# Performance work log

Hardware: AMD Instinct MI355X
Metric: run time of the kernel (lower is better)

The kernel has to match this reference:

```python
import jax, jax.numpy as jnp
import numpy as np

B, N, C, H, D = 1, 256, 128, 4, 32  # batch, n_res, rep2d channels, heads, head dim


def setup_inputs() -> dict:
    key = jax.random.key(0)
    ks = jax.random.split(key, 8)
    r = lambda k, sh: jax.random.normal(k, sh, jnp.float32) * 0.02
    return {
        "x2d": jax.random.normal(ks[0], (B, N, N, C), jnp.float32),
        "norm_w": jnp.ones((C,), jnp.float32),
        "norm_b": jnp.zeros((C,), jnp.float32),
        "wq": r(ks[1], (H * D, C)),
        "wk": r(ks[2], (H * D, C)),
        "wv": r(ks[3], (H * D, C)),
        "wb": r(ks[4], (H, C)),
        "wg": r(ks[5], (H * D, C)),
        "bg": jnp.zeros((H * D,), jnp.float32),
        "wo": r(ks[6], (C, H * D)),
        "bo": jnp.zeros((C,), jnp.float32),
    }


def reference(x2d, norm_w, norm_b, wq, wk, wv, wb, wg, bg, wo, bo):
    # ending_node=False -> no transpose
    mu = jnp.mean(x2d, axis=-1, keepdims=True)
    var = jnp.var(x2d, axis=-1, keepdims=True)
    x = (x2d - mu) * jax.lax.rsqrt(var + 1e-5) * norm_w + norm_b  # LayerNorm

    q = (x @ wq.T).reshape(B, N, N, H, D)
    k = (x @ wk.T).reshape(B, N, N, H, D)
    v = (x @ wv.T).reshape(B, N, N, H, D)

    factor = 1.0 / np.sqrt(D)
    aff = jnp.einsum('bmihd,bmjhd->bmhij', q * factor, k)  # [B,M,H,I,J]

    bias = (x @ wb.T).transpose(0, 3, 1, 2)  # [B,H,I,J]
    # torch `aff + bias` broadcasts bias over the row dim m (valid since B==1)
    weights = jax.nn.softmax(aff + bias[:, None], axis=-1)

    g = jax.nn.sigmoid(x @ wg.T + bg).reshape(B, N, N, H, D)
    out = jnp.einsum('bmhqk,bmkhd->bmqhd', weights, v) * g  # gated per-head output
    out = out.reshape(B, N, N, H * D) @ wo.T + bo
    return out
```

## Files before the change

kernel.cpp:

```cpp
#include <hip/hip_runtime.h>
#include <hip/hip_bf16.h>

#define NRES 256
#define CH   128
#define NH   4
#define HD   32
#define NPX  (NRES*NRES)
#define BPX  64
#define LOG2E 1.4426950408889634f

typedef __hip_bfloat16 bf16;
typedef __attribute__((ext_vector_type(8))) short bf16x8;
typedef __attribute__((ext_vector_type(4))) float f32x4;
typedef __attribute__((ext_vector_type(16))) float f32x16;
typedef __attribute__((ext_vector_type(2))) unsigned int uint2v;

__device__ __forceinline__ float lo_f(unsigned u) { return __uint_as_float(u << 16); }
__device__ __forceinline__ float hi_f(unsigned u) { return __uint_as_float(u & 0xffff0000u); }
__device__ __forceinline__ float fexp2(float x) { return __builtin_amdgcn_exp2f(x); }
__device__ __forceinline__ unsigned pk2(float a, float b) {
    unsigned short ua = __bfloat16_as_ushort(__float2bfloat16(a));
    unsigned short ub = __bfloat16_as_ushort(__float2bfloat16(b));
    return (unsigned)ua | ((unsigned)ub << 16);
}

__global__ __launch_bounds__(256) void prep_kernel(const float* __restrict__ wq,
                                                   const float* __restrict__ wk,
                                                   const float* __restrict__ wv,
                                                   const float* __restrict__ wg,
                                                   const float* __restrict__ wo,
                                                   bf16* __restrict__ dst) {
    int mat = blockIdx.x >> 4;
    int off = ((blockIdx.x & 15) * 256 + threadIdx.x) * 4;
    const float* srcs[5] = {wq, wk, wv, wg, wo};
    float4 v4 = *reinterpret_cast<const float4*>(srcs[mat] + off);
    uint2 o;
    o.x = pk2(v4.x, v4.y);
    o.y = pk2(v4.z, v4.w);
    *reinterpret_cast<uint2*>(dst + (size_t)mat * 16384 + off) = o;
}

__global__ __launch_bounds__(256) void proj_kernel(const float* __restrict__ x2d,
                                                   const float* __restrict__ nw,
                                                   const float* __restrict__ nb,
                                                   const bf16* __restrict__ wgt,
                                                   const float* __restrict__ bg,
                                                   const float* __restrict__ wb,
                                                   bf16* __restrict__ q,
                                                   bf16* __restrict__ k,
                                                   bf16* __restrict__ v,
                                                   bf16* __restrict__ g,
                                                   float* __restrict__ bias) {
    __shared__ short xsb[BPX][128];
    int t = threadIdx.x;
    size_t pbase = (size_t)blockIdx.x * BPX;
    int px = t >> 2, lo = t & 3;

    const float* xrow = x2d + (pbase + px) * CH;
    float4 v4[8];
    #pragma unroll
    for (int cc = 0; cc < 8; ++cc)
        v4[cc] = *reinterpret_cast<const float4*>(xrow + 16 * cc + 4 * lo);

    float s = 0.f, ss = 0.f;
    #pragma unroll
    for (int cc = 0; cc < 8; ++cc) {
        s  += v4[cc].x + v4[cc].y + v4[cc].z + v4[cc].w;
        ss += v4[cc].x * v4[cc].x + v4[cc].y * v4[cc].y
            + v4[cc].z * v4[cc].z + v4[cc].w * v4[cc].w;
    }
    s += __shfl_xor(s, 1); ss += __shfl_xor(ss, 1);
    s += __shfl_xor(s, 2); ss += __shfl_xor(ss, 2);
    float mu  = s * (1.0f / CH);
    float var = ss * (1.0f / CH) - mu * mu;
    float rs  = rsqrtf(var + 1e-5f);

    #pragma unroll
    for (int cc = 0; cc < 8; ++cc) {
        int c0 = 16 * cc + 4 * lo;
        float4 wv = *reinterpret_cast<const float4*>(nw + c0);
        float4 bv = *reinterpret_cast<const float4*>(nb + c0);
        v4[cc].x = (v4[cc].x - mu) * rs * wv.x + bv.x;
        v4[cc].y = (v4[cc].y - mu) * rs * wv.y + bv.y;
        v4[cc].z = (v4[cc].z - mu) * rs * wv.z + bv.z;
        v4[cc].w = (v4[cc].w - mu) * rs * wv.w + bv.w;
        int sc = ((((c0 >> 3) ^ px) & 7) << 3) | (c0 & 7) | (c0 & 64);
        uint2 pw;
        pw.x = pk2(v4[cc].x, v4[cc].y);
        pw.y = pk2(v4[cc].z, v4[cc].w);
        *reinterpret_cast<uint2*>(&xsb[px][sc]) = pw;
    }

    float bp0 = 0.f, bp1 = 0.f, bp2 = 0.f, bp3 = 0.f;
    #pragma unroll
    for (int cc = 0; cc < 8; ++cc) {
        int c0 = 16 * cc + 4 * lo;
        float4 w0 = *reinterpret_cast<const float4*>(wb + 0 * CH + c0);
        float4 w1 = *reinterpret_cast<const float4*>(wb + 1 * CH + c0);
        float4 w2 = *reinterpret_cast<const float4*>(wb + 2 * CH + c0);
        float4 w3 = *reinterpret_cast<const float4*>(wb + 3 * CH + c0);
        bp0 += v4[cc].x * w0.x + v4[cc].y * w0.y + v4[cc].z * w0.z + v4[cc].w * w0.w;
        bp1 += v4[cc].x * w1.x + v4[cc].y * w1.y + v4[cc].z * w1.z + v4[cc].w * w1.w;
        bp2 += v4[cc].x * w2.x + v4[cc].y * w2.y + v4[cc].z * w2.z + v4[cc].w * w2.w;
        bp3 += v4[cc].x * w3.x + v4[cc].y * w3.y + v4[cc].z * w3.z + v4[cc].w * w3.w;
    }
    bp0 += __shfl_xor(bp0, 1); bp0 += __shfl_xor(bp0, 2);
    bp1 += __shfl_xor(bp1, 1); bp1 += __shfl_xor(bp1, 2);
    bp2 += __shfl_xor(bp2, 1); bp2 += __shfl_xor(bp2, 2);
    bp3 += __shfl_xor(bp3, 1); bp3 += __shfl_xor(bp3, 2);
    {
        float bv = (lo == 0) ? bp0 : (lo == 1) ? bp1 : (lo == 2) ? bp2 : bp3;
        bias[(size_t)lo * NPX + pbase + px] = bv * LOG2E;
    }
    __syncthreads();

    int w  = t >> 6, l = t & 63;
    int ll = l & 15, lg = l >> 4;
    bf16* Os[4] = {q, k, v, g};
    const float qscale = 0.17677669529663689f * LOG2E;

    #pragma unroll
    for (int mat = 0; mat < 4; ++mat) {
        const bf16* W = wgt + (size_t)mat * 16384;
        bf16x8 bfr[2][4];
        #pragma unroll
        for (int p = 0; p < 2; ++p)
            #pragma unroll
            for (int kt = 0; kt < 4; ++kt)
                bfr[p][kt] = *reinterpret_cast<const bf16x8*>(
                    W + (size_t)((2 * w + p) * 16 + ll) * CH + kt * 32 + lg * 8);

        f32x4 acc[4][2];
        #pragma unroll
        for (int mt = 0; mt < 4; ++mt)
            #pragma unroll
            for (int p = 0; p < 2; ++p) acc[mt][p] = (f32x4){0.f, 0.f, 0.f, 0.f};

        #pragma unroll
        for (int kt = 0; kt < 4; ++kt) {
            bf16x8 a[4];
            #pragma unroll
            for (int mt = 0; mt < 4; ++mt) {
                int row = 16 * mt + ll;
                int gr  = (kt * 4 + lg) ^ (row & 7);
                a[mt] = *reinterpret_cast<const bf16x8*>(&xsb[row][gr * 8]);
            }
            #pragma unroll
            for (int mt = 0; mt < 4; ++mt)
                #pragma unroll
                for (int p = 0; p < 2; ++p)
                    acc[mt][p] = __builtin_amdgcn_mfma_f32_16x16x32_bf16(a[mt], bfr[p][kt], acc[mt][p], 0, 0, 0);
        }

        #pragma unroll
        for (int p = 0; p < 2; ++p) {
            int o = (2 * w + p) * 16 + ll;
            float bgv = (mat == 3) ? bg[o] : 0.f;
            #pragma unroll
            for (int mt = 0; mt < 4; ++mt) {
                #pragma unroll
                for (int r = 0; r < 4; ++r) {
                    int prow = 16 * mt + lg * 4 + r;
                    float valf = acc[mt][p][r];
                    if (mat == 0) valf *= qscale;
                    if (mat == 3) valf = 1.f / (1.f + __expf(-(valf + bgv)));
                    Os[mat][(pbase + prow) * CH + o] = __float2bfloat16(valf);
                }
            }
        }
    }
}

__global__ __launch_bounds__(256, 4) void attn_kernel(const bf16* q,
                                                      const bf16* __restrict__ kk,
                                                      const bf16* __restrict__ vv,
                                                      const float* __restrict__ bias,
                                                      const bf16* __restrict__ gg,
                                                      bf16* attn) {
    __shared__ short kl[NRES][HD];
    __shared__ short vt[HD][NRES];

    int t   = threadIdx.x;
    int w   = t >> 6;
    int l   = t & 63;
    int l31 = l & 31;
    int hi5 = l >> 5;
    int m = blockIdx.x, h = blockIdx.y;
    size_t base = ((size_t)m * NRES) * CH + (size_t)h * HD;

    for (int it = 0; it < 4; ++it) {
        int e8 = t + 256 * it;
        int j  = e8 >> 2;
        int g  = e8 & 3;
        int d0 = g * 8;
        uint4 ku = *reinterpret_cast<const uint4*>(kk + base + (size_t)j * CH + d0);
        *reinterpret_cast<uint4*>(&kl[j][(g ^ (j & 3) ^ ((j >> 2) & 3)) * 8]) = ku;
        uint4 vu = *reinterpret_cast<const uint4*>(vv + base + (size_t)j * CH + d0);
        union { uint4 u; short s[8]; } vc; vc.u = vu;
        #pragma unroll
        for (int s = 0; s < 8; ++s)
            vt[d0 + s][j ^ (8 * s)] = vc.s[s];
    }

    bf16x8 qf[2][2];
    #pragma unroll
    for (int ig = 0; ig < 2; ++ig)
        #pragma unroll
        for (int tt = 0; tt < 2; ++tt)
            qf[ig][tt] = *reinterpret_cast<const bf16x8*>(
                q + base + (size_t)(w * 64 + ig * 32 + l31) * CH + tt * 16 + hi5 * 8);

    __syncthreads();

    float m_run[2] = {-1e30f, -1e30f};
    float l_run[2] = {0.f, 0.f};
    f32x16 oacc[2];
    #pragma unroll
    for (int ig = 0; ig < 2; ++ig)
        #pragma unroll
        for (int r = 0; r < 16; ++r) oacc[ig][r] = 0.f;

    const float* bh = bias + (size_t)h * NPX;

    for (int jt = 0; jt < 8; ++jt) {
        int j0 = jt * 32;
        int jr = j0 + l31;
        int ksw = (jr & 3) ^ ((jr >> 2) & 3);

        bf16x8 kf0 = *reinterpret_cast<const bf16x8*>(&kl[jr][(hi5 ^ ksw) * 8]);
        bf16x8 kf1 = *reinterpret_cast<const bf16x8*>(&kl[jr][((2 + hi5) ^ ksw) * 8]);

        f32x16 sac[2];
        #pragma unroll
        for (int ig = 0; ig < 2; ++ig) {
            f32x16 zz;
            #pragma unroll
            for (int r = 0; r < 16; ++r) zz[r] = 0.f;
            zz = __builtin_amdgcn_mfma_f32_32x32x16_bf16(kf0, qf[ig][0], zz, 0, 0, 0);
            sac[ig] = __builtin_amdgcn_mfma_f32_32x32x16_bf16(kf1, qf[ig][1], zz, 0, 0, 0);
        }

        __builtin_amdgcn_s_setprio(1);
        #pragma unroll
        for (int ig = 0; ig < 2; ++ig) {
            int i = w * 64 + ig * 32 + l31;
            #pragma unroll
            for (int rq = 0; rq < 4; ++rq) {
                float4 b4 = *reinterpret_cast<const float4*>(bh + (size_t)i * NRES + j0 + 8 * rq + 4 * hi5);
                sac[ig][4 * rq + 0] += b4.x; sac[ig][4 * rq + 1] += b4.y;
                sac[ig][4 * rq + 2] += b4.z; sac[ig][4 * rq + 3] += b4.w;
            }
        }
        __builtin_amdgcn_s_setprio(0);

        #pragma unroll
        for (int ig = 0; ig < 2; ++ig) {
            float a0 = fmaxf(sac[ig][0], sac[ig][1]),  a1 = fmaxf(sac[ig][2], sac[ig][3]);
            float a2 = fmaxf(sac[ig][4], sac[ig][5]),  a3 = fmaxf(sac[ig][6], sac[ig][7]);
            float a4 = fmaxf(sac[ig][8], sac[ig][9]),  a5 = fmaxf(sac[ig][10], sac[ig][11]);
            float a6 = fmaxf(sac[ig][12], sac[ig][13]), a7 = fmaxf(sac[ig][14], sac[ig][15]);
            float mx = fmaxf(fmaxf(fmaxf(a0, a1), fmaxf(a2, a3)), fmaxf(fmaxf(a4, a5), fmaxf(a6, a7)));
            mx = fmaxf(mx, __shfl_xor(mx, 32));

            if (!__all(mx <= m_run[ig] + 8.f)) {
                float mnew = fmaxf(m_run[ig], mx);
                float sc = fexp2(m_run[ig] - mnew);
                l_run[ig] *= sc;
                #pragma unroll
                for (int r = 0; r < 16; ++r) oacc[ig][r] *= sc;
                m_run[ig] = mnew;
            }
            float mm = m_run[ig];
            #pragma unroll
            for (int r = 0; r < 16; ++r) sac[ig][r] = fexp2(sac[ig][r] - mm);
            float s0 = sac[ig][0] + sac[ig][1],  s1 = sac[ig][2] + sac[ig][3];
            float s2 = sac[ig][4] + sac[ig][5],  s3 = sac[ig][6] + sac[ig][7];
            float s4 = sac[ig][8] + sac[ig][9],  s5 = sac[ig][10] + sac[ig][11];
            float s6 = sac[ig][12] + sac[ig][13], s7 = sac[ig][14] + sac[ig][15];
            float psum = ((s0 + s1) + (s2 + s3)) + ((s4 + s5) + (s6 + s7));
            psum += __shfl_xor(psum, 32);
            l_run[ig] += psum;
        }

        __builtin_amdgcn_s_setprio(1);
        #pragma unroll
        for (int tt = 0; tt < 2; ++tt) {
            bf16x8 vf = *reinterpret_cast<const bf16x8*>(
                &vt[l31][(j0 + 16 * tt + 8 * hi5) ^ (8 * (l31 & 7))]);
            #pragma unroll
            for (int ig = 0; ig < 2; ++ig) {
                unsigned x0 = pk2(sac[ig][8 * tt + 0], sac[ig][8 * tt + 1]);
                unsigned x1 = pk2(sac[ig][8 * tt + 2], sac[ig][8 * tt + 3]);
                unsigned y0 = pk2(sac[ig][8 * tt + 4], sac[ig][8 * tt + 5]);
                unsigned y1 = pk2(sac[ig][8 * tt + 6], sac[ig][8 * tt + 7]);
                uint2v r0 = __builtin_amdgcn_permlane32_swap(x0, y0, false, false);
                uint2v r1 = __builtin_amdgcn_permlane32_swap(x1, y1, false, false);
                union { unsigned u[4]; bf16x8 v; } pf;
                pf.u[0] = r0[0];
                pf.u[1] = r1[0];
                pf.u[2] = r0[1];
                pf.u[3] = r1[1];
                oacc[ig] = __builtin_amdgcn_mfma_f32_32x32x16_bf16(vf, pf.v, oacc[ig], 0, 0, 0);
            }
        }
        __builtin_amdgcn_s_setprio(0);
    }

    #pragma unroll
    for (int ig = 0; ig < 2; ++ig) {
        float inv = 1.f / l_run[ig];
        size_t prow = base + (size_t)(w * 64 + ig * 32 + l31) * CH;
        #pragma unroll
        for (int rq = 0; rq < 4; ++rq) {
            int d0 = 8 * rq + 4 * hi5;
            uint2 gu = *reinterpret_cast<const uint2*>(gg + prow + d0);
            float g0 = lo_f(gu.x), g1 = hi_f(gu.x), g2 = lo_f(gu.y), g3 = hi_f(gu.y);
            uint2 ow;
            ow.x = pk2(oacc[ig][4 * rq + 0] * inv * g0, oacc[ig][4 * rq + 1] * inv * g1);
            ow.y = pk2(oacc[ig][4 * rq + 2] * inv * g2, oacc[ig][4 * rq + 3] * inv * g3);
            *reinterpret_cast<uint2*>(attn + prow + d0) = ow;
        }
    }
}

__global__ __launch_bounds__(256) void out_kernel(const bf16* __restrict__ ga,
                                                  const bf16* __restrict__ wob,
                                                  const float* __restrict__ bo,
                                                  float* __restrict__ out) {
    __shared__ short xsb[BPX][128];
    int t = threadIdx.x;
    size_t pbase = (size_t)blockIdx.x * BPX;

    for (int it = 0; it < 4; ++it) {
        int idx = (it * 256 + t) * 8;
        int px = idx >> 7, c = idx & 127;
        int gr = c >> 3;
        uint4 u = *reinterpret_cast<const uint4*>(ga + pbase * CH + idx);
        *reinterpret_cast<uint4*>(&xsb[px][(gr ^ (px & 7)) * 8]) = u;
    }
    __syncthreads();

    int w  = t >> 6, l = t & 63;
    int ll = l & 15, lg = l >> 4;

    bf16x8 bfr[2][4];
    #pragma unroll
    for (int p = 0; p < 2; ++p)
        #pragma unroll
        for (int kt = 0; kt < 4; ++kt)
            bfr[p][kt] = *reinterpret_cast<const bf16x8*>(
                wob + (size_t)((2 * w + p) * 16 + ll) * CH + kt * 32 + lg * 8);

    f32x4 acc[4][2];
    #pragma unroll
    for (int mt = 0; mt < 4; ++mt)
        #pragma unroll
        for (int p = 0; p < 2; ++p) acc[mt][p] = (f32x4){0.f, 0.f, 0.f, 0.f};

    #pragma unroll
    for (int kt = 0; kt < 4; ++kt) {
        bf16x8 a[4];
        #pragma unroll
        for (int mt = 0; mt < 4; ++mt) {
            int row = 16 * mt + ll;
            int gr  = (kt * 4 + lg) ^ (row & 7);
            a[mt] = *reinterpret_cast<const bf16x8*>(&xsb[row][gr * 8]);
        }
        #pragma unroll
        for (int mt = 0; mt < 4; ++mt)
            #pragma unroll
            for (int p = 0; p < 2; ++p)
                acc[mt][p] = __builtin_amdgcn_mfma_f32_16x16x32_bf16(a[mt], bfr[p][kt], acc[mt][p], 0, 0, 0);
    }

    #pragma unroll
    for (int p = 0; p < 2; ++p) {
        int o = (2 * w + p) * 16 + ll;
        float bov = bo[o];
        #pragma unroll
        for (int mt = 0; mt < 4; ++mt)
            #pragma unroll
            for (int r = 0; r < 4; ++r) {
                int prow = 16 * mt + lg * 4 + r;
                out[(pbase + prow) * CH + o] = acc[mt][p][r] + bov;
            }
    }
}

extern "C" void kernel_launch(void* const* d_in, const int* in_sizes, int n_in,
                              void* d_out, int out_size, void* d_ws, size_t ws_size,
                              hipStream_t stream) {
    const float* x2d = (const float*)d_in[0];
    const float* nw  = (const float*)d_in[1];
    const float* nb  = (const float*)d_in[2];
    const float* wq  = (const float*)d_in[3];
    const float* wk  = (const float*)d_in[4];
    const float* wv  = (const float*)d_in[5];
    const float* wb  = (const float*)d_in[6];
    const float* wg  = (const float*)d_in[7];
    const float* bg  = (const float*)d_in[8];
    const float* wo  = (const float*)d_in[9];
    const float* bo  = (const float*)d_in[10];
    float* out = (float*)d_out;

    float* bias = (float*)d_ws;
    bf16*  q    = (bf16*)((float*)d_ws + (size_t)NH * NPX);
    bf16*  k    = q + (size_t)NPX * CH;
    bf16*  v    = k + (size_t)NPX * CH;
    bf16*  g    = v + (size_t)NPX * CH;
    bf16*  wgt  = g + (size_t)NPX * CH;
    bf16*  wob  = wgt + 4 * 16384;

    prep_kernel<<<80, 256, 0, stream>>>(wq, wk, wv, wg, wo, wgt);
    proj_kernel<<<NPX / BPX, 256, 0, stream>>>(x2d, nw, nb, wgt, bg, wb, q, k, v, g, bias);
    attn_kernel<<<dim3(NRES, NH), 256, 0, stream>>>(q, k, v, bias, g, q);
    out_kernel<<<NPX / BPX, 256, 0, stream>>>(q, wob, bo, out);
}
```

Before: 103.6 us.

## Pre-transpose pair bias into i-contiguous tiles for coalesced attention loads

Adds a small kernel that rearranges the per-head pair bias into blocks of 32 rows stored j-major with i contiguous, so that in the attention loop lanes indexed by i read consecutive floats. Before, each lane read float4s from a different row (strided by 256 floats), which gave poorly coalesced bias fetches repeated across all 256 m-blocks. The cost is an extra kernel launch plus a 1 MB read and write. The change also lowers the occupancy hint from 4 to 3 waves and drops the setprio around the bias loads.

Measured after the change: 92.33 us. -10.9%, faster.

```diff
diff --git a/kernel.cpp b/kernel.cpp
--- a/kernel.cpp
+++ b/kernel.cpp
@@ -171,10 +171,36 @@
     }
 }
 
-__global__ __launch_bounds__(256, 4) void attn_kernel(const bf16* q,
+__global__ __launch_bounds__(256) void ibias_kernel(const float* __restrict__ bias,
+                                                    float* __restrict__ biasI) {
+    __shared__ float tile[32][65];
+    int h   = blockIdx.x >> 5;
+    int g32 = (blockIdx.x >> 2) & 7;
+    int jt4 = blockIdx.x & 3;
+    int t   = threadIdx.x;
+
+    const float* src = bias + (size_t)h * NPX + (size_t)(g32 * 32) * NRES + jt4 * 64;
+    int jr = t & 63, ir = t >> 6;
+    #pragma unroll
+    for (int it = 0; it < 8; ++it) {
+        int i = ir + 4 * it;
+        tile[i][jr] = src[(size_t)i * NRES + jr];
+    }
+    __syncthreads();
+
+    float* dst = biasI + ((size_t)(h * 8 + g32) * NRES + jt4 * 64) * 32;
+    int i5 = t & 31, jw = t >> 5;
+    #pragma unroll
+    for (int it = 0; it < 8; ++it) {
+        int j = jw + 8 * it;
+        dst[(size_t)j * 32 + i5] = tile[i5][j];
+    }
+}
+
+__global__ __launch_bounds__(256, 3) void attn_kernel(const bf16* q,
                                                       const bf16* __restrict__ kk,
                                                       const bf16* __restrict__ vv,
-                                                      const float* __restrict__ bias,
+                                                      const float* __restrict__ biasI,
                                                       const bf16* __restrict__ gg,
                                                       bf16* attn) {
     __shared__ short kl[NRES][HD];
@@ -220,7 +246,7 @@
         #pragma unroll
         for (int r = 0; r < 16; ++r) oacc[ig][r] = 0.f;
 
-    const float* bh = bias + (size_t)h * NPX;
+    const float* bI0 = biasI + ((size_t)(h * 8 + 2 * w) * NRES) * 32 + l31;
 
     for (int jt = 0; jt < 8; ++jt) {
         int j0 = jt * 32;
@@ -240,18 +266,15 @@
             sac[ig] = __builtin_amdgcn_mfma_f32_32x32x16_bf16(kf1, qf[ig][1], zz, 0, 0, 0);
         }
 
-        __builtin_amdgcn_s_setprio(1);
         #pragma unroll
         for (int ig = 0; ig < 2; ++ig) {
-            int i = w * 64 + ig * 32 + l31;
-            #pragma unroll
-            for (int rq = 0; rq < 4; ++rq) {
-                float4 b4 = *reinterpret_cast<const float4*>(bh + (size_t)i * NRES + j0 + 8 * rq + 4 * hi5);
-                sac[ig][4 * rq + 0] += b4.x; sac[ig][4 * rq + 1] += b4.y;
-                sac[ig][4 * rq + 2] += b4.z; sac[ig][4 * rq + 3] += b4.w;
-            }
-        }
-        __builtin_amdgcn_s_setprio(0);
+            const float* bp = bI0 + (size_t)ig * (NRES * 32) + (size_t)j0 * 32;
+            #pragma unroll
+            for (int r = 0; r < 16; ++r) {
+                int jl = (r & 3) + 8 * (r >> 2) + 4 * hi5;
+                sac[ig][r] += bp[(size_t)jl * 32];
+            }
+        }
 
         #pragma unroll
         for (int ig = 0; ig < 2; ++ig) {
@@ -410,9 +433,11 @@
     bf16*  g    = v + (size_t)NPX * CH;
     bf16*  wgt  = g + (size_t)NPX * CH;
     bf16*  wob  = wgt + 4 * 16384;
+    float* biasI = (float*)(wob + 16384);
 
     prep_kernel<<<80, 256, 0, stream>>>(wq, wk, wv, wg, wo, wgt);
     proj_kernel<<<NPX / BPX, 256, 0, stream>>>(x2d, nw, nb, wgt, bg, wb, q, k, v, g, bias);
-    attn_kernel<<<dim3(NRES, NH), 256, 0, stream>>>(q, k, v, bias, g, q);
+    ibias_kernel<<<128, 256, 0, stream>>>(bias, biasI);
+    attn_kernel<<<dim3(NRES, NH), 256, 0, stream>>>(q, k, v, biasI, g, q);
     out_kernel<<<NPX / BPX, 256, 0, stream>>>(q, wob, bo, out);
 }
```
